# Optimization experiments

Hardware: AMD Instinct MI355X
Metric: run time of the kernel (lower is better)

Reference implementation:

```python
import jax, jax.numpy as jnp
import numpy as np

B, S, D = 32, 4096, 2048

def setup_inputs() -> dict:
    key = jax.random.key(0)
    k1, k2 = jax.random.split(key)
    decoder_hidden = jax.random.normal(k1, (B, D), dtype=jnp.float32)
    encoder_states = jax.random.normal(k2, (B, S, D), dtype=jnp.float32)
    return {"decoder_hidden": decoder_hidden, "encoder_states": encoder_states}

def reference(decoder_hidden, encoder_states):
    # scores: [B, S] = encoder_states @ decoder_hidden (per batch)
    scores = jnp.einsum('bsd,bd->bs', encoder_states, decoder_hidden)
    # softmax over the sequence dim (torch Softmax(dim=1) on [B, S, 1])
    attn = jax.nn.softmax(scores, axis=1)
    # weighted sum of encoder states: [B, D]
    return jnp.einsum('bs,bsd->bd', attn, encoder_states)
```

## Files before the change

kernel.cpp:

```cpp
#include <hip/hip_runtime.h>
#include <math.h>

namespace {

constexpr int kB = 32;
constexpr int kS = 4096;
constexpr int kD = 2048;
constexpr int kNW = 4;

__global__ __launch_bounds__(256, 2)
void attn_partial(const float* __restrict__ h,
                  const float* __restrict__ E,
                  float* __restrict__ acc_ws,
                  float* __restrict__ ml_ws,
                  int nchunk)
{
    const int c    = blockIdx.x;
    const int b    = blockIdx.y;
    const int t    = threadIdx.x;
    const int lane = t & 63;
    const int wave = t >> 6;
    const int cs   = kS / nchunk;
    const int s0   = c * cs;
    const int P    = cs / kNW / 2;

    const float* hb = h + (size_t)b * kD;
    float4 hreg[8];
#pragma unroll
    for (int k = 0; k < 8; ++k)
        hreg[k] = *reinterpret_cast<const float4*>(hb + 256 * k + 4 * lane);

    float4 acc[8];
#pragma unroll
    for (int k = 0; k < 8; ++k) acc[k] = make_float4(0.f, 0.f, 0.f, 0.f);
    float m = -INFINITY, l = 0.f;

    const float* Eb = E + ((size_t)b * kS + s0 + wave) * kD + 4 * lane;

    float4 e0a[8], e0b[8], e1a[8], e1b[8];

#define LOADP(ra, rb, j)                                                     \
    {                                                                        \
        const float* _r0 = Eb + (size_t)(2 * (j)) * (kNW * kD);              \
        const float* _r1 = _r0 + (kNW * kD);                                 \
        _Pragma("unroll")                                                    \
        for (int k = 0; k < 8; ++k) {                                        \
            ra[k] = *reinterpret_cast<const float4*>(_r0 + 256 * k);         \
            rb[k] = *reinterpret_cast<const float4*>(_r1 + 256 * k);         \
        }                                                                    \
    }

#define COMPP(ra, rb)                                                        \
    {                                                                        \
        float pa = 0.f, pb = 0.f;                                            \
        _Pragma("unroll")                                                    \
        for (int k = 0; k < 8; ++k) {                                        \
            pa += ra[k].x * hreg[k].x + ra[k].y * hreg[k].y +                \
                  ra[k].z * hreg[k].z + ra[k].w * hreg[k].w;                 \
            pb += rb[k].x * hreg[k].x + rb[k].y * hreg[k].y +                \
                  rb[k].z * hreg[k].z + rb[k].w * hreg[k].w;                 \
        }                                                                    \
        _Pragma("unroll")                                                    \
        for (int off = 32; off > 0; off >>= 1) {                             \
            pa += __shfl_xor(pa, off, 64);                                   \
            pb += __shfl_xor(pb, off, 64);                                   \
        }                                                                    \
        const float mnew = fmaxf(m, fmaxf(pa, pb));              \
        if (mnew > m) {                              \
            const float scale = __expf(m - mnew);                            \
            _Pragma("unroll")                                                \
            for (int k = 0; k < 8; ++k) {                                    \
                acc[k].x *= scale; acc[k].y *= scale;                        \
                acc[k].z *= scale; acc[k].w *= scale;                        \
            }                                                                \
            l *= scale;                                                      \
            m = mnew;                                                        \
        }                                                                    \
        const float wa = __expf(pa - m);                                     \
        const float wb = __expf(pb - m);                                     \
        l += wa + wb;                                                        \
        _Pragma("unroll")                                                    \
        for (int k = 0; k < 8; ++k) {                                        \
            acc[k].x += wa * ra[k].x + wb * rb[k].x;                         \
            acc[k].y += wa * ra[k].y + wb * rb[k].y;                         \
            acc[k].z += wa * ra[k].z + wb * rb[k].z;                         \
            acc[k].w += wa * ra[k].w + wb * rb[k].w;                         \
        }                                                                    \
    }

    LOADP(e0a, e0b, 0);
    LOADP(e1a, e1b, 1);
    for (int j = 0; j < P - 2; j += 2) {
        COMPP(e0a, e0b);
        LOADP(e0a, e0b, j + 2);
        COMPP(e1a, e1b);
        LOADP(e1a, e1b, j + 3);
    }
    COMPP(e0a, e0b);
    COMPP(e1a, e1b);

#undef LOADP
#undef COMPP

    float* aout = acc_ws + (((size_t)b * nchunk + c) * kNW + wave) * kD;
#pragma unroll
    for (int k = 0; k < 8; ++k)
        *reinterpret_cast<float4*>(aout + 256 * k + 4 * lane) = acc[k];
    if (lane == 0) {
        float* ml = ml_ws + (((size_t)b * nchunk + c) * kNW + wave) * 2;
        ml[0] = m;
        ml[1] = l;
    }
}

__global__ __launch_bounds__(64)
void attn_combine(const float* __restrict__ acc_ws,
                  const float* __restrict__ ml_ws,
                  float* __restrict__ out,
                  int np)
{
    const int slice = blockIdx.x;
    const int b     = blockIdx.y;
    const int t     = threadIdx.x;
    const int col   = slice * 256 + 4 * t;

    const float* ml = ml_ws + (size_t)b * np * 2;
    float M = -INFINITY;
    for (int p = 0; p < np; ++p) M = fmaxf(M, ml[2 * p]);

    float L = 0.f;
    float4 o = {0.f, 0.f, 0.f, 0.f};
    for (int p = 0; p < np; ++p) {
        const float coef = __expf(ml[2 * p] - M);
        L += ml[2 * p + 1] * coef;
        const float4 a = *reinterpret_cast<const float4*>(
            acc_ws + ((size_t)b * np + p) * kD + col);
        o.x += coef * a.x; o.y += coef * a.y;
        o.z += coef * a.z; o.w += coef * a.w;
    }
    const float inv = 1.f / L;
    float4 r = {o.x * inv, o.y * inv, o.z * inv, o.w * inv};
    *reinterpret_cast<float4*>(out + (size_t)b * kD + col) = r;
}

}

extern "C" void kernel_launch(void* const* d_in, const int* in_sizes, int n_in,
                              void* d_out, int out_size, void* d_ws, size_t ws_size,
                              hipStream_t stream) {
    const float* h = (const float*)d_in[0];
    const float* E = (const float*)d_in[1];
    float* out = (float*)d_out;

    int nchunk = 16;
    while (nchunk > 1 &&
           (size_t)kB * nchunk * kNW * (kD + 2) * sizeof(float) > ws_size)
        nchunk >>= 1;

    float* acc_ws = (float*)d_ws;
    float* ml_ws  = acc_ws + (size_t)kB * nchunk * kNW * kD;

    dim3 g1(nchunk, kB);
    attn_partial<<<g1, 256, 0, stream>>>(h, E, acc_ws, ml_ws, nchunk);
    dim3 g2(kD / 256, kB);
    attn_combine<<<g2, 64, 0, stream>>>(acc_ws, ml_ws, out, nchunk * kNW);
}
```

Before: 210.8 us.

## Merge per-wave partials in LDS, use nontemporal loads and vector math

The four waves' online-softmax partials are now merged inside each block through shared memory in a two-step tree reduction. Each block writes one partial per chunk instead of four, which cuts workspace traffic and the combine kernel's loop count by a factor of four. Encoder loads are marked nontemporal to avoid polluting the cache, since the encoder tensor is streamed once. Dot products and accumulates are rewritten with ext_vector_type math. The cost is extra LDS use and barriers at the tail of the partial kernel.

```diff
diff --git a/kernel.cpp b/kernel.cpp
--- a/kernel.cpp
+++ b/kernel.cpp
@@ -7,6 +7,8 @@
 constexpr int kS = 4096;
 constexpr int kD = 2048;
 constexpr int kNW = 4;
+
+typedef float v4f __attribute__((ext_vector_type(4)));
 
 __global__ __launch_bounds__(256, 2)
 void attn_partial(const float* __restrict__ h,
@@ -24,20 +26,23 @@
     const int s0   = c * cs;
     const int P    = cs / kNW / 2;
 
+    __shared__ v4f   sh_merge[2][512];
+    __shared__ float sh_ml[2][2];
+
     const float* hb = h + (size_t)b * kD;
-    float4 hreg[8];
+    v4f hreg[8];
 #pragma unroll
     for (int k = 0; k < 8; ++k)
-        hreg[k] = *reinterpret_cast<const float4*>(hb + 256 * k + 4 * lane);
+        hreg[k] = *reinterpret_cast<const v4f*>(hb + 256 * k + 4 * lane);
 
-    float4 acc[8];
+    v4f acc[8];
 #pragma unroll
-    for (int k = 0; k < 8; ++k) acc[k] = make_float4(0.f, 0.f, 0.f, 0.f);
+    for (int k = 0; k < 8; ++k) acc[k] = (v4f)(0.f);
     float m = -INFINITY, l = 0.f;
 
     const float* Eb = E + ((size_t)b * kS + s0 + wave) * kD + 4 * lane;
 
-    float4 e0a[8], e0b[8], e1a[8], e1b[8];
+    v4f e0a[8], e0b[8], e1a[8], e1b[8];
 
 #define LOADP(ra, rb, j)                                                     \
     {                                                                        \
@@ -45,21 +50,23 @@
         const float* _r1 = _r0 + (kNW * kD);                                 \
         _Pragma("unroll")                                                    \
         for (int k = 0; k < 8; ++k) {                                        \
-            ra[k] = *reinterpret_cast<const float4*>(_r0 + 256 * k);         \
-            rb[k] = *reinterpret_cast<const float4*>(_r1 + 256 * k);         \
+            ra[k] = __builtin_nontemporal_load(                              \
+                reinterpret_cast<const v4f*>(_r0 + 256 * k));                \
+            rb[k] = __builtin_nontemporal_load(                              \
+                reinterpret_cast<const v4f*>(_r1 + 256 * k));                \
         }                                                                    \
     }
 
 #define COMPP(ra, rb)                                                        \
     {                                                                        \
-        float pa = 0.f, pb = 0.f;                                            \
+        v4f va = (v4f)(0.f), vb = (v4f)(0.f);                                \
         _Pragma("unroll")                                                    \
         for (int k = 0; k < 8; ++k) {                                        \
-            pa += ra[k].x * hreg[k].x + ra[k].y * hreg[k].y +                \
-                  ra[k].z * hreg[k].z + ra[k].w * hreg[k].w;                 \
-            pb += rb[k].x * hreg[k].x + rb[k].y * hreg[k].y +                \
-                  rb[k].z * hreg[k].z + rb[k].w * hreg[k].w;                 \
+            va += ra[k] * hreg[k];                                           \
+            vb += rb[k] * hreg[k];                                           \
         }                                                                    \
+        float pa = va.x + va.y + va.z + va.w;                                \
+        float pb = vb.x + vb.y + vb.z + vb.w;                                \
         _Pragma("unroll")                                                    \
         for (int off = 32; off > 0; off >>= 1) {                             \
             pa += __shfl_xor(pa, off, 64);                                   \
@@ -69,10 +76,7 @@
         if (mnew > m) {                              \
             const float scale = __expf(m - mnew);                            \
             _Pragma("unroll")                                                \
-            for (int k = 0; k < 8; ++k) {                                    \
-                acc[k].x *= scale; acc[k].y *= scale;                        \
-                acc[k].z *= scale; acc[k].w *= scale;                        \
-            }                                                                \
+            for (int k = 0; k < 8; ++k) acc[k] *= scale;                     \
             l *= scale;                                                      \
             m = mnew;                                                        \
         }                                                                    \
@@ -80,12 +84,8 @@
         const float wb = __expf(pb - m);                                     \
         l += wa + wb;                                                        \
         _Pragma("unroll")                                                    \
-        for (int k = 0; k < 8; ++k) {                                        \
-            acc[k].x += wa * ra[k].x + wb * rb[k].x;                         \
-            acc[k].y += wa * ra[k].y + wb * rb[k].y;                         \
-            acc[k].z += wa * ra[k].z + wb * rb[k].z;                         \
-            acc[k].w += wa * ra[k].w + wb * rb[k].w;                         \
-        }                                                                    \
+        for (int k = 0; k < 8; ++k)                                          \
+            acc[k] += wa * ra[k] + wb * rb[k];                               \
     }
 
     LOADP(e0a, e0b, 0);
@@ -102,14 +102,44 @@
 #undef LOADP
 #undef COMPP
 
-    float* aout = acc_ws + (((size_t)b * nchunk + c) * kNW + wave) * kD;
+    if (wave >= 2) {
 #pragma unroll
-    for (int k = 0; k < 8; ++k)
-        *reinterpret_cast<float4*>(aout + 256 * k + 4 * lane) = acc[k];
-    if (lane == 0) {
-        float* ml = ml_ws + (((size_t)b * nchunk + c) * kNW + wave) * 2;
-        ml[0] = m;
-        ml[1] = l;
+        for (int k = 0; k < 8; ++k) sh_merge[wave - 2][k * 64 + lane] = acc[k];
+        if (lane == 0) { sh_ml[wave - 2][0] = m; sh_ml[wave - 2][1] = l; }
+    }
+    __syncthreads();
+    if (wave < 2) {
+        const float pm = sh_ml[wave][0], pl = sh_ml[wave][1];
+        const float mnew = fmaxf(m, pm);
+        const float sa = __expf(m - mnew), sb = __expf(pm - mnew);
+#pragma unroll
+        for (int k = 0; k < 8; ++k)
+            acc[k] = acc[k] * sa + sh_merge[wave][k * 64 + lane] * sb;
+        l = l * sa + pl * sb;
+        m = mnew;
+    }
+    __syncthreads();
+    if (wave == 1) {
+#pragma unroll
+        for (int k = 0; k < 8; ++k) sh_merge[0][k * 64 + lane] = acc[k];
+        if (lane == 0) { sh_ml[0][0] = m; sh_ml[0][1] = l; }
+    }
+    __syncthreads();
+    if (wave == 0) {
+        const float pm = sh_ml[0][0], pl = sh_ml[0][1];
+        const float mnew = fmaxf(m, pm);
+        const float sa = __expf(m - mnew), sb = __expf(pm - mnew);
+        float* aout = acc_ws + ((size_t)b * nchunk + c) * kD;
+#pragma unroll
+        for (int k = 0; k < 8; ++k) {
+            v4f r = acc[k] * sa + sh_merge[0][k * 64 + lane] * sb;
+            *reinterpret_cast<v4f*>(aout + 256 * k + 4 * lane) = r;
+        }
+        if (lane == 0) {
+            float* ml = ml_ws + ((size_t)b * nchunk + c) * 2;
+            ml[0] = mnew;
+            ml[1] = l * sa + pl * sb;
+        }
     }
 }
 
@@ -129,18 +159,17 @@
     for (int p = 0; p < np; ++p) M = fmaxf(M, ml[2 * p]);
 
     float L = 0.f;
-    float4 o = {0.f, 0.f, 0.f, 0.f};
+    v4f o = (v4f)(0.f);
     for (int p = 0; p < np; ++p) {
         const float coef = __expf(ml[2 * p] - M);
         L += ml[2 * p + 1] * coef;
-        const float4 a = *reinterpret_cast<const float4*>(
+        const v4f a = *reinterpret_cast<const v4f*>(
             acc_ws + ((size_t)b * np + p) * kD + col);
-        o.x += coef * a.x; o.y += coef * a.y;
-        o.z += coef * a.z; o.w += coef * a.w;
+        o += coef * a;
     }
     const float inv = 1.f / L;
-    float4 r = {o.x * inv, o.y * inv, o.z * inv, o.w * inv};
-    *reinterpret_cast<float4*>(out + (size_t)b * kD + col) = r;
+    v4f r = o * inv;
+    *reinterpret_cast<v4f*>(out + (size_t)b * kD + col) = r;
 }
 
 }
@@ -154,14 +183,14 @@
 
     int nchunk = 16;
     while (nchunk > 1 &&
-           (size_t)kB * nchunk * kNW * (kD + 2) * sizeof(float) > ws_size)
+           (size_t)kB * nchunk * (kD + 2) * sizeof(float) > ws_size)
         nchunk >>= 1;
 
     float* acc_ws = (float*)d_ws;
-    float* ml_ws  = acc_ws + (size_t)kB * nchunk * kNW * kD;
+    float* ml_ws  = acc_ws + (size_t)kB * nchunk * kD;
 
     dim3 g1(nchunk, kB);
     attn_partial<<<g1, 256, 0, stream>>>(h, E, acc_ws, ml_ws, nchunk);
     dim3 g2(kD / 256, kB);
-    attn_combine<<<g2, 64, 0, stream>>>(acc_ws, ml_ws, out, nchunk * kNW);
+    attn_combine<<<g2, 64, 0, stream>>>(acc_ws, ml_ws, out, nchunk);
 }
```

After: 168.8 us. 19.9% less time.
